# Performance work log

Measured on AMD Instinct MI355X. Metric: run time of the kernel, lower is better.

Reference implementation:

```python
import jax, jax.numpy as jnp
import numpy as np

B, T, C, HS = 512, 256, 384, 64  # batch, block_size, n_embed, head_size


def setup_inputs() -> dict:
    key = jax.random.key(0)
    kx, kq, kk, kv = jax.random.split(key, 4)
    x = jax.random.normal(kx, (B, T, C), dtype=jnp.float32)
    # Linear(n_embed, head_size, bias=False) weights stored as [in, out]
    s = 1.0 / np.sqrt(C)
    Wq = jax.random.normal(kq, (C, HS), dtype=jnp.float32) * s
    Wk = jax.random.normal(kk, (C, HS), dtype=jnp.float32) * s
    Wv = jax.random.normal(kv, (C, HS), dtype=jnp.float32) * s
    return {"x": x, "Wq": Wq, "Wk": Wk, "Wv": Wv}


def reference(x, Wq, Wk, Wv):
    Bb, Tt, Cc = x.shape
    q = jnp.einsum('btc,ch->bth', x, Wq)
    k = jnp.einsum('btc,ch->bth', x, Wk)
    v = jnp.einsum('btc,ch->bth', x, Wv)
    # NOTE: original scales by C**-0.5 (embed dim), NOT head_size**-0.5
    wei = jnp.einsum('bqh,bkh->bqk', q, k) * (Cc ** -0.5)
    # causal mask: tril == 0 (strict upper triangle) -> -inf
    causal = jnp.tril(jnp.ones((Tt, Tt), dtype=bool))
    wei = jnp.where(causal[None, :, :], wei, -jnp.inf)
    # NOTE: original applies softmax over dim=1 (query axis) — replicated faithfully
    wei = jax.nn.softmax(wei, axis=1)
    out = jnp.einsum('bqk,bkh->bqh', wei, v)
    return out
```

## Files before the change

kernel.cpp:

```cpp
#include <hip/hip_runtime.h>

typedef float  f32x4  __attribute__((ext_vector_type(4)));
typedef __bf16 bf16x8 __attribute__((ext_vector_type(8)));

#define CC 384
#define AS1 __attribute__((address_space(1)))
#define AS3 __attribute__((address_space(3)))

__device__ __forceinline__ unsigned short f2bf(float f) {
  union { float f; unsigned int u; } x; x.f = f;
  unsigned int u = x.u;
  return (unsigned short)((u + 0x7fffu + ((u >> 16) & 1u)) >> 16);
}

__device__ __forceinline__ f32x4 mfma16(bf16x8 a, bf16x8 b, f32x4 c) {
  return __builtin_amdgcn_mfma_f32_16x16x32_bf16(a, b, c, 0, 0, 0);
}

__global__ void repack_w(const float* __restrict__ Wq, const float* __restrict__ Wk,
                         const float* __restrict__ Wv, unsigned short* __restrict__ wf) {
  int e = blockIdx.x * 512 + threadIdx.x;
  int k = e / 192;
  int n = e - k * 192;
  const float* W = (n < 64) ? Wq : (n < 128) ? Wk : Wv;
  float val = W[k * 64 + (n & 63)];
  int kk = k >> 5;
  int lane = (((k >> 3) & 3) << 4) | (n & 15);
  int j = k & 7;
  int nt = n >> 4;
  wf[(size_t)(((kk * 12 + nt) << 6) + lane) * 8 + j] = f2bf(val);
}

__global__ __launch_bounds__(512, 2) void fused(const float* __restrict__ x,
                                                const unsigned short* __restrict__ wf,
                                                float* __restrict__ out) {
  __shared__ __attribute__((aligned(16))) unsigned char smem[119808];
  unsigned short (*Sx)[72] = (unsigned short(*)[72])smem;
  unsigned short (*kL)[72] = (unsigned short(*)[72])(smem + 36864);
  unsigned short (*vT)[264] = (unsigned short(*)[264])(smem + 73728);
  float* pm = (float*)(smem + 107520);
  float* ps = pm + 1024;
  float* gg = ps + 1024;
  unsigned short* wst = (unsigned short*)smem;

  const int tid = threadIdx.x;
  const int w = tid >> 6, lane = tid & 63;
  const int l15 = lane & 15, lhi = lane >> 4;
  const int b = blockIdx.x;
  const int mts[2] = {w, 15 - w};

  const float* xr0 = x + ((size_t)b * 256 + mts[0] * 16 + l15) * CC + lhi * 8;
  const float* xr1 = x + ((size_t)b * 256 + mts[1] * 16 + l15) * CC + lhi * 8;

  f32x4 zero = {0.f, 0.f, 0.f, 0.f};
  f32x4 acc[2][12];
#pragma unroll
  for (int i = 0; i < 2; ++i)
#pragma unroll
    for (int nt = 0; nt < 12; ++nt) acc[i][nt] = zero;

  f32x4 xreg[2][8];

#define WSTAGE(kp_, b_) do {                                                                  \
    const unsigned short* s_ = wf + (size_t)(kp_) * 12288 + tid * 8;                          \
    unsigned short* d_ = wst + (b_) * 12288 + tid * 8;                                        \
    __builtin_amdgcn_global_load_lds((const AS1 void*)(s_),        (AS3 void*)(d_),        16, 0, 0); \
    __builtin_amdgcn_global_load_lds((const AS1 void*)(s_ + 4096), (AS3 void*)(d_ + 4096), 16, 0, 0); \
    __builtin_amdgcn_global_load_lds((const AS1 void*)(s_ + 8192), (AS3 void*)(d_ + 8192), 16, 0, 0); \
  } while (0)
#define XLOAD(kp_, s_) do {                                                                   \
    const int o_ = (kp_) * 64;                                                                \
    xreg[s_][0] = *(const f32x4*)(xr0 + o_);      xreg[s_][1] = *(const f32x4*)(xr0 + o_ + 4);  \
    xreg[s_][2] = *(const f32x4*)(xr0 + o_ + 32); xreg[s_][3] = *(const f32x4*)(xr0 + o_ + 36); \
    xreg[s_][4] = *(const f32x4*)(xr1 + o_);      xreg[s_][5] = *(const f32x4*)(xr1 + o_ + 4);  \
    xreg[s_][6] = *(const f32x4*)(xr1 + o_ + 32); xreg[s_][7] = *(const f32x4*)(xr1 + o_ + 36); \
  } while (0)

  WSTAGE(0, 0);
  WSTAGE(1, 1);
  XLOAD(0, 0);
  __builtin_amdgcn_sched_barrier(0);
  asm volatile("s_waitcnt vmcnt(11)" ::: "memory");
  __builtin_amdgcn_s_barrier();
  __builtin_amdgcn_sched_barrier(0);

#pragma unroll
  for (int kp = 0; kp < 6; ++kp) {
    const int cur = kp & 1, nxt = cur ^ 1;
    if (kp < 5) XLOAD(kp + 1, nxt);
    if (kp < 4) WSTAGE(kp + 2, (kp + 2) % 3);
    __builtin_amdgcn_sched_barrier(0);
    const unsigned short* base = wst + (kp % 3) * 12288;
#pragma unroll
    for (int i = 0; i < 2; ++i) {
#pragma unroll
      for (int k2 = 0; k2 < 2; ++k2) {
        bf16x8 af;
#pragma unroll
        for (int j = 0; j < 4; ++j) {
          af[j]     = (__bf16)xreg[cur][i * 4 + k2 * 2][j];
          af[4 + j] = (__bf16)xreg[cur][i * 4 + k2 * 2 + 1][j];
        }
        const bf16x8* bp = (const bf16x8*)(base + k2 * 6144) + lane;
#pragma unroll
        for (int nt = 0; nt < 12; ++nt) acc[i][nt] = mfma16(af, bp[nt * 64], acc[i][nt]);
      }
    }
    __builtin_amdgcn_sched_barrier(0);
    if (kp < 4)       asm volatile("s_waitcnt vmcnt(11)" ::: "memory");
    else if (kp == 4) asm volatile("s_waitcnt vmcnt(8)" ::: "memory");
    if (kp < 5) {
      __builtin_amdgcn_s_barrier();
      __builtin_amdgcn_sched_barrier(0);
    }
  }
#undef WSTAGE
#undef XLOAD
  __syncthreads();

  const float qs = 0.05103103630798288f;
#pragma unroll
  for (int i = 0; i < 2; ++i) {
    const int rb = mts[i] * 16 + lhi * 4;
#pragma unroll
    for (int nt = 0; nt < 4; ++nt) {
      const int h = nt * 16 + l15;
#pragma unroll
      for (int r = 0; r < 4; ++r) Sx[rb + r][h] = f2bf(acc[i][nt][r] * qs);
    }
#pragma unroll
    for (int nt = 4; nt < 8; ++nt) {
      const int h = (nt - 4) * 16 + l15;
#pragma unroll
      for (int r = 0; r < 4; ++r) kL[rb + r][h] = f2bf(acc[i][nt][r]);
    }
#pragma unroll
    for (int nt = 8; nt < 12; ++nt) {
      const int h = (nt - 8) * 16 + l15;
      unsigned long long pk =
          (unsigned long long)f2bf(acc[i][nt][0]) |
          ((unsigned long long)f2bf(acc[i][nt][1]) << 16) |
          ((unsigned long long)f2bf(acc[i][nt][2]) << 32) |
          ((unsigned long long)f2bf(acc[i][nt][3]) << 48);
      *(unsigned long long*)&vT[h][rb] = pk;
    }
  }
  __syncthreads();

  bf16x8 qf[2][2];
#pragma unroll
  for (int i = 0; i < 2; ++i)
#pragma unroll
    for (int kk = 0; kk < 2; ++kk)
      qf[i][kk] = *(const bf16x8*)&Sx[mts[i] * 16 + l15][kk * 32 + lhi * 8];

  f32x4 oacc[2][4];
#pragma unroll
  for (int i = 0; i < 2; ++i)
#pragma unroll
    for (int nh = 0; nh < 4; ++nh) oacc[i][nh] = zero;

  for (int p = 0; p < 4; ++p) {
    const int p4 = 4 * p;
    const bool any = (mts[1] >= p4);
    if (any) {
      bf16x8 kf[4][2];
#pragma unroll
      for (int c = 0; c < 4; ++c)
#pragma unroll
        for (int kk = 0; kk < 2; ++kk)
          kf[c][kk] = *(const bf16x8*)&kL[p * 64 + c * 16 + l15][kk * 32 + lhi * 8];
#pragma unroll
      for (int i = 0; i < 2; ++i) {
        const int mt = mts[i];
        if (mt < p4) continue;
        const int cmax = mt - p4;
        const int rowb = mt * 16 + lhi * 4;
#pragma unroll
        for (int c = 0; c < 4; ++c) {
          const int cs = c * 16 + l15;
          if (c <= cmax) {
            f32x4 s = zero;
            s = mfma16(qf[i][0], kf[c][0], s);
            s = mfma16(qf[i][1], kf[c][1], s);
            const int cg = p * 64 + cs;
            const bool v0 = (rowb + 0) >= cg, v1 = (rowb + 1) >= cg;
            const bool v2 = (rowb + 2) >= cg, v3 = (rowb + 3) >= cg;
            float m = -1e30f;
            m = fmaxf(m, v0 ? s[0] : -1e30f);
            m = fmaxf(m, v1 ? s[1] : -1e30f);
            m = fmaxf(m, v2 ? s[2] : -1e30f);
            m = fmaxf(m, v3 ? s[3] : -1e30f);
            m = fmaxf(m, __shfl_xor(m, 16));
            m = fmaxf(m, __shfl_xor(m, 32));
            const float e0 = v0 ? __expf(s[0] - m) : 0.f;
            const float e1 = v1 ? __expf(s[1] - m) : 0.f;
            const float e2 = v2 ? __expf(s[2] - m) : 0.f;
            const float e3 = v3 ? __expf(s[3] - m) : 0.f;
            float t = e0 + e1 + e2 + e3;
            t += __shfl_xor(t, 16);
            t += __shfl_xor(t, 32);
            Sx[rowb + 0][cs] = f2bf(e0);
            Sx[rowb + 1][cs] = f2bf(e1);
            Sx[rowb + 2][cs] = f2bf(e2);
            Sx[rowb + 3][cs] = f2bf(e3);
            if (lhi == 0) { pm[mt * 64 + cs] = m; ps[mt * 64 + cs] = t; }
          } else {
            if (lhi == 0) { pm[mt * 64 + cs] = -1e30f; ps[mt * 64 + cs] = 0.f; }
          }
        }
      }
    }
    __syncthreads();
    {
      float M = -1e30f;
      for (int mt = p4; mt < 16; ++mt) M = fmaxf(M, pm[mt * 64 + lane]);
      float L = 0.f;
      for (int mt = p4; mt < 16; ++mt) L += ps[mt * 64 + lane] * __expf(pm[mt * 64 + lane] - M);
      const float rv = 1.0f / L;
      int mtw = p4 + w;
      if (mtw < 16) gg[mtw * 64 + lane] = __expf(pm[mtw * 64 + lane] - M) * rv;
      mtw += 8;
      if (mtw < 16) gg[mtw * 64 + lane] = __expf(pm[mtw * 64 + lane] - M) * rv;
    }
    __syncthreads();
    if (any) {
      bf16x8 vf[4][2];
#pragma unroll
      for (int nh = 0; nh < 4; ++nh)
#pragma unroll
        for (int kk = 0; kk < 2; ++kk)
          vf[nh][kk] = *(const bf16x8*)&vT[nh * 16 + l15][p * 64 + kk * 32 + lhi * 8];
#pragma unroll
      for (int i = 0; i < 2; ++i) {
        const int mt = mts[i];
        if (mt < p4) continue;
        const int grow = mt * 16 + l15;
        const int dmax = mt - p4;
#pragma unroll
        for (int kk = 0; kk < 2; ++kk) {
          if (kk == 1 && dmax <= 1) continue;
          const int c0 = kk * 32 + lhi * 8;
          bf16x8 se = *(const bf16x8*)&Sx[grow][c0];
          f32x4 gA = *(const f32x4*)&gg[mt * 64 + c0];
          f32x4 gB = *(const f32x4*)&gg[mt * 64 + c0 + 4];
          const int cg0 = p * 64 + c0;
          bf16x8 wfr;
#pragma unroll
          for (int j = 0; j < 4; ++j)
            wfr[j] = (cg0 + j <= grow) ? (__bf16)((float)se[j] * gA[j]) : (__bf16)0.f;
#pragma unroll
          for (int j = 0; j < 4; ++j)
            wfr[4 + j] = (cg0 + 4 + j <= grow) ? (__bf16)((float)se[4 + j] * gB[j]) : (__bf16)0.f;
#pragma unroll
          for (int nh = 0; nh < 4; ++nh) oacc[i][nh] = mfma16(wfr, vf[nh][kk], oacc[i][nh]);
        }
      }
    }
  }
#pragma unroll
  for (int i = 0; i < 2; ++i) {
    const int rb = mts[i] * 16 + lhi * 4;
#pragma unroll
    for (int nh = 0; nh < 4; ++nh) {
      const int h = nh * 16 + l15;
#pragma unroll
      for (int r = 0; r < 4; ++r)
        out[(size_t)b * 16384 + (size_t)(rb + r) * 64 + h] = oacc[i][nh][r];
    }
  }
}

extern "C" void kernel_launch(void* const* d_in, const int* in_sizes, int n_in,
                              void* d_out, int out_size, void* d_ws, size_t ws_size,
                              hipStream_t stream) {
  const float* x  = (const float*)d_in[0];
  const float* Wq = (const float*)d_in[1];
  const float* Wk = (const float*)d_in[2];
  const float* Wv = (const float*)d_in[3];
  float* out = (float*)d_out;

  unsigned short* wf = (unsigned short*)d_ws;

  repack_w<<<144, 512, 0, stream>>>(Wq, Wk, Wv, wf);
  fused<<<512, 512, 0, stream>>>(x, wf, out);
}
```

Measured before the change: 91.63 us.

## Use 1024-thread blocks with per-wave row tiles and split column halves

Doubles the workgroup to 16 waves. In the projection GEMM each wave now owns one 16-row tile instead of two, which halves accumulator registers. In the attention phase, waves pair on the same query tiles and split the key columns and head dimensions between two halves. The hand-tuned triple-buffered weight staging with explicit vmcnt waits is replaced by simpler double buffering with a __syncthreads each step. This also adds extra barriers in the attention loop, trading pipelining control for more waves per block to hide latency. The bound of 4 blocks per CU cannot be met with about 117 KB of LDS per block, so residency falls to one block per CU (16 waves).

```diff
diff --git a/kernel.cpp b/kernel.cpp
--- a/kernel.cpp
+++ b/kernel.cpp
@@ -31,9 +31,9 @@
   wf[(size_t)(((kk * 12 + nt) << 6) + lane) * 8 + j] = f2bf(val);
 }
 
-__global__ __launch_bounds__(512, 2) void fused(const float* __restrict__ x,
-                                                const unsigned short* __restrict__ wf,
-                                                float* __restrict__ out) {
+__global__ __launch_bounds__(1024, 4) void fused(const float* __restrict__ x,
+                                                 const unsigned short* __restrict__ wf,
+                                                 float* __restrict__ out) {
   __shared__ __attribute__((aligned(16))) unsigned char smem[119808];
   unsigned short (*Sx)[72] = (unsigned short(*)[72])smem;
   unsigned short (*kL)[72] = (unsigned short(*)[72])(smem + 36864);
@@ -47,101 +47,82 @@
   const int w = tid >> 6, lane = tid & 63;
   const int l15 = lane & 15, lhi = lane >> 4;
   const int b = blockIdx.x;
-  const int mts[2] = {w, 15 - w};
-
-  const float* xr0 = x + ((size_t)b * 256 + mts[0] * 16 + l15) * CC + lhi * 8;
-  const float* xr1 = x + ((size_t)b * 256 + mts[1] * 16 + l15) * CC + lhi * 8;
+  const int u = w & 7, chalf = w >> 3;
+  const int mts[2] = {u, 15 - u};
+
+  const float* xr = x + ((size_t)b * 256 + w * 16 + l15) * CC + lhi * 8;
 
   f32x4 zero = {0.f, 0.f, 0.f, 0.f};
-  f32x4 acc[2][12];
-#pragma unroll
-  for (int i = 0; i < 2; ++i)
-#pragma unroll
-    for (int nt = 0; nt < 12; ++nt) acc[i][nt] = zero;
-
-  f32x4 xreg[2][8];
+  f32x4 acc[12];
+#pragma unroll
+  for (int nt = 0; nt < 12; ++nt) acc[nt] = zero;
 
 #define WSTAGE(kp_, b_) do {                                                                  \
     const unsigned short* s_ = wf + (size_t)(kp_) * 12288 + tid * 8;                          \
     unsigned short* d_ = wst + (b_) * 12288 + tid * 8;                                        \
-    __builtin_amdgcn_global_load_lds((const AS1 void*)(s_),        (AS3 void*)(d_),        16, 0, 0); \
-    __builtin_amdgcn_global_load_lds((const AS1 void*)(s_ + 4096), (AS3 void*)(d_ + 4096), 16, 0, 0); \
-    __builtin_amdgcn_global_load_lds((const AS1 void*)(s_ + 8192), (AS3 void*)(d_ + 8192), 16, 0, 0); \
+    __builtin_amdgcn_global_load_lds((const AS1 void*)(s_), (AS3 void*)(d_), 16, 0, 0);       \
+    if (tid < 512)                                                                            \
+      __builtin_amdgcn_global_load_lds((const AS1 void*)(s_ + 8192), (AS3 void*)(d_ + 8192),  \
+                                       16, 0, 0);                                             \
   } while (0)
-#define XLOAD(kp_, s_) do {                                                                   \
+#define XLOAD(kp_, a_) do {                                                                   \
     const int o_ = (kp_) * 64;                                                                \
-    xreg[s_][0] = *(const f32x4*)(xr0 + o_);      xreg[s_][1] = *(const f32x4*)(xr0 + o_ + 4);  \
-    xreg[s_][2] = *(const f32x4*)(xr0 + o_ + 32); xreg[s_][3] = *(const f32x4*)(xr0 + o_ + 36); \
-    xreg[s_][4] = *(const f32x4*)(xr1 + o_);      xreg[s_][5] = *(const f32x4*)(xr1 + o_ + 4);  \
-    xreg[s_][6] = *(const f32x4*)(xr1 + o_ + 32); xreg[s_][7] = *(const f32x4*)(xr1 + o_ + 36); \
+    a_[0][0] = *(const f32x4*)(xr + o_);      a_[0][1] = *(const f32x4*)(xr + o_ + 4);        \
+    a_[1][0] = *(const f32x4*)(xr + o_ + 32); a_[1][1] = *(const f32x4*)(xr + o_ + 36);       \
   } while (0)
 
   WSTAGE(0, 0);
-  WSTAGE(1, 1);
-  XLOAD(0, 0);
-  __builtin_amdgcn_sched_barrier(0);
-  asm volatile("s_waitcnt vmcnt(11)" ::: "memory");
-  __builtin_amdgcn_s_barrier();
-  __builtin_amdgcn_sched_barrier(0);
-
-#pragma unroll
+  f32x4 aC[2][2];
+  XLOAD(0, aC);
+
   for (int kp = 0; kp < 6; ++kp) {
-    const int cur = kp & 1, nxt = cur ^ 1;
-    if (kp < 5) XLOAD(kp + 1, nxt);
-    if (kp < 4) WSTAGE(kp + 2, (kp + 2) % 3);
-    __builtin_amdgcn_sched_barrier(0);
-    const unsigned short* base = wst + (kp % 3) * 12288;
-#pragma unroll
-    for (int i = 0; i < 2; ++i) {
-#pragma unroll
-      for (int k2 = 0; k2 < 2; ++k2) {
-        bf16x8 af;
-#pragma unroll
-        for (int j = 0; j < 4; ++j) {
-          af[j]     = (__bf16)xreg[cur][i * 4 + k2 * 2][j];
-          af[4 + j] = (__bf16)xreg[cur][i * 4 + k2 * 2 + 1][j];
-        }
-        const bf16x8* bp = (const bf16x8*)(base + k2 * 6144) + lane;
-#pragma unroll
-        for (int nt = 0; nt < 12; ++nt) acc[i][nt] = mfma16(af, bp[nt * 64], acc[i][nt]);
-      }
-    }
-    __builtin_amdgcn_sched_barrier(0);
-    if (kp < 4)       asm volatile("s_waitcnt vmcnt(11)" ::: "memory");
-    else if (kp == 4) asm volatile("s_waitcnt vmcnt(8)" ::: "memory");
+    __syncthreads();
+    f32x4 aN[2][2];
+#pragma unroll
+    for (int k2 = 0; k2 < 2; ++k2) { aN[k2][0] = zero; aN[k2][1] = zero; }
     if (kp < 5) {
-      __builtin_amdgcn_s_barrier();
-      __builtin_amdgcn_sched_barrier(0);
-    }
+      XLOAD(kp + 1, aN);
+      WSTAGE(kp + 1, (kp + 1) & 1);
+    }
+#pragma unroll
+    for (int k2 = 0; k2 < 2; ++k2) {
+      bf16x8 af;
+#pragma unroll
+      for (int j = 0; j < 4; ++j) { af[j] = (__bf16)aC[k2][0][j]; af[4 + j] = (__bf16)aC[k2][1][j]; }
+      const bf16x8* bp = (const bf16x8*)(wst + (kp & 1) * 12288 + k2 * 6144) + lane;
+#pragma unroll
+      for (int nt = 0; nt < 12; ++nt) acc[nt] = mfma16(af, bp[nt * 64], acc[nt]);
+    }
+#pragma unroll
+    for (int k2 = 0; k2 < 2; ++k2) { aC[k2][0] = aN[k2][0]; aC[k2][1] = aN[k2][1]; }
   }
 #undef WSTAGE
 #undef XLOAD
   __syncthreads();
 
   const float qs = 0.05103103630798288f;
-#pragma unroll
-  for (int i = 0; i < 2; ++i) {
-    const int rb = mts[i] * 16 + lhi * 4;
+  {
+    const int rb = w * 16 + lhi * 4;
 #pragma unroll
     for (int nt = 0; nt < 4; ++nt) {
       const int h = nt * 16 + l15;
 #pragma unroll
-      for (int r = 0; r < 4; ++r) Sx[rb + r][h] = f2bf(acc[i][nt][r] * qs);
+      for (int r = 0; r < 4; ++r) Sx[rb + r][h] = f2bf(acc[nt][r] * qs);
     }
 #pragma unroll
     for (int nt = 4; nt < 8; ++nt) {
       const int h = (nt - 4) * 16 + l15;
 #pragma unroll
-      for (int r = 0; r < 4; ++r) kL[rb + r][h] = f2bf(acc[i][nt][r]);
+      for (int r = 0; r < 4; ++r) kL[rb + r][h] = f2bf(acc[nt][r]);
     }
 #pragma unroll
     for (int nt = 8; nt < 12; ++nt) {
       const int h = (nt - 8) * 16 + l15;
       unsigned long long pk =
-          (unsigned long long)f2bf(acc[i][nt][0]) |
-          ((unsigned long long)f2bf(acc[i][nt][1]) << 16) |
-          ((unsigned long long)f2bf(acc[i][nt][2]) << 32) |
-          ((unsigned long long)f2bf(acc[i][nt][3]) << 48);
+          (unsigned long long)f2bf(acc[nt][0]) |
+          ((unsigned long long)f2bf(acc[nt][1]) << 16) |
+          ((unsigned long long)f2bf(acc[nt][2]) << 32) |
+          ((unsigned long long)f2bf(acc[nt][3]) << 48);
       *(unsigned long long*)&vT[h][rb] = pk;
     }
   }
@@ -153,23 +134,26 @@
 #pragma unroll
     for (int kk = 0; kk < 2; ++kk)
       qf[i][kk] = *(const bf16x8*)&Sx[mts[i] * 16 + l15][kk * 32 + lhi * 8];
-
-  f32x4 oacc[2][4];
+  __syncthreads();
+
+  f32x4 oacc[2][2];
 #pragma unroll
   for (int i = 0; i < 2; ++i)
 #pragma unroll
-    for (int nh = 0; nh < 4; ++nh) oacc[i][nh] = zero;
+    for (int nh2 = 0; nh2 < 2; ++nh2) oacc[i][nh2] = zero;
 
   for (int p = 0; p < 4; ++p) {
     const int p4 = 4 * p;
     const bool any = (mts[1] >= p4);
     if (any) {
-      bf16x8 kf[4][2];
-#pragma unroll
-      for (int c = 0; c < 4; ++c)
+      bf16x8 kf[2][2];
+#pragma unroll
+      for (int c2 = 0; c2 < 2; ++c2) {
+        const int c = chalf * 2 + c2;
 #pragma unroll
         for (int kk = 0; kk < 2; ++kk)
-          kf[c][kk] = *(const bf16x8*)&kL[p * 64 + c * 16 + l15][kk * 32 + lhi * 8];
+          kf[c2][kk] = *(const bf16x8*)&kL[p * 64 + c * 16 + l15][kk * 32 + lhi * 8];
+      }
 #pragma unroll
       for (int i = 0; i < 2; ++i) {
         const int mt = mts[i];
@@ -177,12 +161,13 @@
         const int cmax = mt - p4;
         const int rowb = mt * 16 + lhi * 4;
 #pragma unroll
-        for (int c = 0; c < 4; ++c) {
+        for (int c2 = 0; c2 < 2; ++c2) {
+          const int c = chalf * 2 + c2;
           const int cs = c * 16 + l15;
           if (c <= cmax) {
             f32x4 s = zero;
-            s = mfma16(qf[i][0], kf[c][0], s);
-            s = mfma16(qf[i][1], kf[c][1], s);
+            s = mfma16(qf[i][0], kf[c2][0], s);
+            s = mfma16(qf[i][1], kf[c2][1], s);
             const int cg = p * 64 + cs;
             const bool v0 = (rowb + 0) >= cg, v1 = (rowb + 1) >= cg;
             const bool v2 = (rowb + 2) >= cg, v3 = (rowb + 3) >= cg;
@@ -218,19 +203,17 @@
       float L = 0.f;
       for (int mt = p4; mt < 16; ++mt) L += ps[mt * 64 + lane] * __expf(pm[mt * 64 + lane] - M);
       const float rv = 1.0f / L;
-      int mtw = p4 + w;
+      const int mtw = p4 + w;
       if (mtw < 16) gg[mtw * 64 + lane] = __expf(pm[mtw * 64 + lane] - M) * rv;
-      mtw += 8;
-      if (mtw < 16) gg[mtw * 64 + lane] = __expf(pm[mtw * 64 + lane] - M) * rv;
     }
     __syncthreads();
     if (any) {
-      bf16x8 vf[4][2];
-#pragma unroll
-      for (int nh = 0; nh < 4; ++nh)
+      bf16x8 vf[2][2];
+#pragma unroll
+      for (int nh2 = 0; nh2 < 2; ++nh2)
 #pragma unroll
         for (int kk = 0; kk < 2; ++kk)
-          vf[nh][kk] = *(const bf16x8*)&vT[nh * 16 + l15][p * 64 + kk * 32 + lhi * 8];
+          vf[nh2][kk] = *(const bf16x8*)&vT[(chalf * 2 + nh2) * 16 + l15][p * 64 + kk * 32 + lhi * 8];
 #pragma unroll
       for (int i = 0; i < 2; ++i) {
         const int mt = mts[i];
@@ -253,20 +236,21 @@
           for (int j = 0; j < 4; ++j)
             wfr[4 + j] = (cg0 + 4 + j <= grow) ? (__bf16)((float)se[4 + j] * gB[j]) : (__bf16)0.f;
 #pragma unroll
-          for (int nh = 0; nh < 4; ++nh) oacc[i][nh] = mfma16(wfr, vf[nh][kk], oacc[i][nh]);
+          for (int nh2 = 0; nh2 < 2; ++nh2) oacc[i][nh2] = mfma16(wfr, vf[nh2][kk], oacc[i][nh2]);
         }
       }
     }
+    __syncthreads();
   }
 #pragma unroll
   for (int i = 0; i < 2; ++i) {
     const int rb = mts[i] * 16 + lhi * 4;
 #pragma unroll
-    for (int nh = 0; nh < 4; ++nh) {
-      const int h = nh * 16 + l15;
+    for (int nh2 = 0; nh2 < 2; ++nh2) {
+      const int h = (chalf * 2 + nh2) * 16 + l15;
 #pragma unroll
       for (int r = 0; r < 4; ++r)
-        out[(size_t)b * 16384 + (size_t)(rb + r) * 64 + h] = oacc[i][nh][r];
+        out[(size_t)b * 16384 + (size_t)(rb + r) * 64 + h] = oacc[i][nh2][r];
     }
   }
 }
@@ -283,5 +267,5 @@
   unsigned short* wf = (unsigned short*)d_ws;
 
   repack_w<<<144, 512, 0, stream>>>(Wq, Wk, Wv, wf);
-  fused<<<512, 512, 0, stream>>>(x, wf, out);
-}
+  fused<<<512, 1024, 0, stream>>>(x, wf, out);
+}
```

Result: faster. 86.58 us (-5.5%).
